# Kernel optimization log

Hardware: AMD Instinct MI355X
Metric: run time of the kernel (lower is better)

The kernel has to match this reference:

```python
import jax, jax.numpy as jnp
import numpy as np

N, E, D, L = 100000, 1_600_000, 128, 8


def setup_inputs() -> dict:
    key = jax.random.key(0)
    k0, k1, k2 = jax.random.split(key, 3)
    x = jax.random.normal(k0, (N, D), dtype=jnp.float32)
    edge_index = jax.random.randint(k1, (2, E), 0, N, dtype=jnp.int64)
    Ws = jax.random.normal(k2, (L, D, D), dtype=jnp.float32) / np.float32(np.sqrt(D))
    bs = jnp.zeros((L, D), dtype=jnp.float32)
    return {"x": x, "edge_index": edge_index, "Ws": Ws, "bs": bs}


def _gcn_conv(h, W, b, src, dst, norm_edge, self_norm):
    """PyG GCNConv: linear -> sym-normalized aggregate (with self loops) -> +bias."""
    h = h @ W                                    # [N, D]
    msg = h[src] * norm_edge[:, None]            # [E, D] gather + scale
    agg = jax.ops.segment_sum(msg, dst, num_segments=h.shape[0])  # scatter-add
    return agg + h * self_norm[:, None] + b      # self-loop term fused in


def reference(x, edge_index, Ws, bs):
    src, dst = edge_index[0], edge_index[1]
    # degree of (A + I) on target nodes, symmetric normalization
    deg = jax.ops.segment_sum(jnp.ones((src.shape[0],), jnp.float32), dst,
                              num_segments=x.shape[0]) + 1.0
    dis = deg ** -0.5                            # deg >= 1, safe
    norm_edge = dis[src] * dis[dst]              # per-edge norm
    self_norm = dis * dis                        # per-node self-loop norm

    n_layers = Ws.shape[0]
    h = x
    initial = x
    for i in range(n_layers):
        h = _gcn_conv(h, Ws[i], bs[i], src, dst, norm_edge, self_norm)
        if i > 0:
            h = h + initial
            initial = h
        h = jax.nn.relu(h)
        if i < n_layers - 1:
            # NOTE: at i == 0 the original indexes layers[-1] (last layer) — faithful.
            j = i - 1
            h = h + _gcn_conv(h, Ws[j], bs[j], src, dst, norm_edge, self_norm)
    return h
```

## Files before the change

kernel.cpp:

```cpp
#include <hip/hip_runtime.h>

#define D 128
#define SCAN_CH 1024
#define SA_STRIDE 136
#define SC_STRIDE 132
#define NPB 64
#define CONV_THREADS 512

typedef _Float16 f16x8 __attribute__((ext_vector_type(8)));
typedef _Float16 f16x4 __attribute__((ext_vector_type(4)));
typedef float f32x4 __attribute__((ext_vector_type(4)));


__global__ void hist_kernel(const int* __restrict__ dst, int* __restrict__ counts,
                            int E, int N) {
  int range = blockIdx.x & 7;
  int lo = (int)(((long long)N * range) >> 3);
  int hi = (int)(((long long)N * (range + 1)) >> 3);
  int stride = (gridDim.x >> 3) * blockDim.x;
  for (int e = (blockIdx.x >> 3) * blockDim.x + threadIdx.x; e < E; e += stride) {
    int d = dst[e];
    if (d >= lo && d < hi) atomicAdd(&counts[d], 1);
  }
}

__global__ void fill_kernel(const int* __restrict__ src, const int* __restrict__ dst,
    int* __restrict__ fillp, int* __restrict__ csr_src, int E, int N) {
  int range = blockIdx.x & 7;
  int lo = (int)(((long long)N * range) >> 3);
  int hi = (int)(((long long)N * (range + 1)) >> 3);
  int stride = (gridDim.x >> 3) * blockDim.x;
  for (int e = (blockIdx.x >> 3) * blockDim.x + threadIdx.x; e < E; e += stride) {
    int d = dst[e];
    if (d >= lo && d < hi) {
      int s = src[e];
      int p = atomicAdd(&fillp[d], 1);
      csr_src[p] = s;
    }
  }
}

__global__ void dis_kernel(const int* __restrict__ counts, float2* __restrict__ dnr, int N) {
  int n = blockIdx.x * blockDim.x + threadIdx.x;
  if (n < N) {
    float c = (float)counts[n] + 1.0f;
    dnr[n] = make_float2(rsqrtf(c), sqrtf(c));
  }
}

__global__ __launch_bounds__(256) void scan_phaseA(const int* __restrict__ counts,
    int* __restrict__ blksum, int N) {
  __shared__ int red[256];
  int base = blockIdx.x * SCAN_CH;
  int t = threadIdx.x;
  int s = 0;
  #pragma unroll
  for (int j = 0; j < 4; ++j) {
    int idx = base + t * 4 + j;
    if (idx < N) s += counts[idx];
  }
  red[t] = s;
  __syncthreads();
  for (int d = 128; d > 0; d >>= 1) {
    if (t < d) red[t] += red[t + d];
    __syncthreads();
  }
  if (t == 0) blksum[blockIdx.x] = red[0];
}

__global__ __launch_bounds__(1024) void scan_phaseB(int* __restrict__ blksum, int NB) {
  __shared__ int sa[1024], sb[1024];
  int t = threadIdx.x;
  int v = (t < NB) ? blksum[t] : 0;
  sa[t] = v;
  __syncthreads();
  int* a = sa; int* b = sb;
  for (int d = 1; d < 1024; d <<= 1) {
    int val = a[t] + ((t >= d) ? a[t - d] : 0);
    b[t] = val;
    __syncthreads();
    int* tmp = a; a = b; b = tmp;
  }
  if (t < NB) blksum[t] = a[t] - v;
}

__global__ __launch_bounds__(256) void scan_phaseC(const int* __restrict__ counts,
    const int* __restrict__ blksum, int* __restrict__ row_ptr, int* __restrict__ fillp, int N) {
  __shared__ int ra[256], rb[256];
  int base = blockIdx.x * SCAN_CH;
  int t = threadIdx.x;
  int v[4]; int s = 0;
  #pragma unroll
  for (int j = 0; j < 4; ++j) {
    int idx = base + t * 4 + j;
    v[j] = (idx < N) ? counts[idx] : 0;
    s += v[j];
  }
  ra[t] = s;
  __syncthreads();
  int* a = ra; int* b = rb;
  for (int d = 1; d < 256; d <<= 1) {
    int val = a[t] + ((t >= d) ? a[t - d] : 0);
    b[t] = val;
    __syncthreads();
    int* tmp = a; a = b; b = tmp;
  }
  int excl = a[t] - s + blksum[blockIdx.x];
  #pragma unroll
  for (int j = 0; j < 4; ++j) {
    int idx = base + t * 4 + j;
    if (idx < N) {
      row_ptr[idx] = excl;
      fillp[idx] = excl;
      excl += v[j];
      if (idx == N - 1) row_ptr[N] = excl;
    }
  }
}


__global__ void conv_x_kernel(const float* __restrict__ x, const float2* __restrict__ dnr,
    _Float16* __restrict__ hs, int total8) {
  int i = blockIdx.x * blockDim.x + threadIdx.x;
  if (i >= total8) return;
  int node = i >> 4;
  float dn = dnr[node].x;
  const float4* p = (const float4*)(x + (size_t)i * 8);
  float4 a = p[0], b = p[1];
  f16x8 v;
  v[0] = (_Float16)(dn * a.x); v[1] = (_Float16)(dn * a.y);
  v[2] = (_Float16)(dn * a.z); v[3] = (_Float16)(dn * a.w);
  v[4] = (_Float16)(dn * b.x); v[5] = (_Float16)(dn * b.y);
  v[6] = (_Float16)(dn * b.z); v[7] = (_Float16)(dn * b.w);
  *(f16x8*)(hs + (size_t)i * 8) = v;
}

__global__ void repack_w_kernel(const float* __restrict__ Ws, _Float16* __restrict__ Wf, int total) {
  int t = blockIdx.x * blockDim.x + threadIdx.x;
  if (t >= total) return;
  int lane = t & 63;
  int nb = (t >> 6) & 7;
  int kb = (t >> 9) & 3;
  int l = t >> 11;
  int col = nb * 16 + (lane & 15);
  int k0 = kb * 32 + (lane >> 4) * 8;
  const float* w = Ws + (size_t)l * D * D;
  f16x8 v;
  #pragma unroll
  for (int j = 0; j < 8; ++j) v[j] = (_Float16)w[(k0 + j) * D + col];
  *(f16x8*)(Wf + (size_t)t * 8) = v;
}

__global__ __launch_bounds__(CONV_THREADS) void conv_fused_kernel(
    const _Float16* __restrict__ hs, const int* __restrict__ row_ptr,
    const int* __restrict__ csr_src, const float2* __restrict__ dnr,
    const f16x8* __restrict__ Wf, const float* __restrict__ bias,
    const float* __restrict__ init32, const _Float16* __restrict__ init16in,
    _Float16* __restrict__ init16out, float* __restrict__ out,
    _Float16* __restrict__ hs_out, int N, int flags) {
  __shared__ __align__(16) char smem[NPB * SC_STRIDE * 4];
  _Float16* sA = (_Float16*)smem;
  float* sC = (float*)smem;
  int tid = threadIdx.x;
  int node0 = blockIdx.x * NPB;
  int ng = tid >> 4;
  int li = tid & 15;
  int c0 = li * 8;

  float2 dr[2];
  f16x8 ownr[2];

  #pragma unroll
  for (int k = 0; k < 2; ++k) {
    int lr = ng + 32 * k;
    int n = node0 + lr;
    f16x8 g = {};
    if (n < N) {
      float acc[8];
      #pragma unroll
      for (int j = 0; j < 8; ++j) acc[j] = 0.f;
      int beg = row_ptr[n], end = row_ptr[n + 1];
      #pragma unroll 4
      for (int e = beg; e < end; ++e) {
        int s = csr_src[e];
        f16x8 v = *(const f16x8*)&hs[(size_t)s * D + c0];
        #pragma unroll
        for (int j = 0; j < 8; ++j) acc[j] += (float)v[j];
      }
      f16x8 own = *(const f16x8*)&hs[(size_t)n * D + c0];
      float2 d2 = dnr[n];
      dr[k] = d2;
      ownr[k] = own;
      #pragma unroll
      for (int j = 0; j < 8; ++j) g[j] = (_Float16)(d2.x * (acc[j] + (float)own[j]));
    }
    *(f16x8*)&sA[lr * SA_STRIDE + c0] = g;
  }

  int wave = tid >> 6, lane = tid & 63;
  f16x8 bf[4];
  #pragma unroll
  for (int kb = 0; kb < 4; ++kb)
    bf[kb] = Wf[(kb * 8 + wave) * 64 + lane];
  __syncthreads();

  f32x4 ca[4];
  #pragma unroll
  for (int rt = 0; rt < 4; ++rt) ca[rt] = (f32x4){0, 0, 0, 0};
  #pragma unroll
  for (int rt = 0; rt < 4; ++rt) {
    #pragma unroll
    for (int kb = 0; kb < 4; ++kb) {
      f16x8 a = *(const f16x8*)&sA[(rt * 16 + (lane & 15)) * SA_STRIDE + kb * 32 + (lane >> 4) * 8];
      ca[rt] = __builtin_amdgcn_mfma_f32_16x16x32_f16(a, bf[kb], ca[rt], 0, 0, 0);
    }
  }
  __syncthreads();

  {
    int colb = wave * 16 + (lane & 15);
    int rowb = (lane >> 4) * 4;
    #pragma unroll
    for (int rt = 0; rt < 4; ++rt)
      #pragma unroll
      for (int r = 0; r < 4; ++r)
        sC[(rt * 16 + rowb + r) * SC_STRIDE + colb] = ca[rt][r];
  }
  __syncthreads();

  float4 b0 = *(const float4*)&bias[c0];
  float4 b1 = *(const float4*)&bias[c0 + 4];
  #pragma unroll
  for (int k = 0; k < 2; ++k) {
    int lr = ng + 32 * k;
    int n = node0 + lr;
    if (n >= N) continue;
    float v[8];
    float4 s0 = *(const float4*)&sC[lr * SC_STRIDE + c0];
    float4 s1 = *(const float4*)&sC[lr * SC_STRIDE + c0 + 4];
    v[0] = s0.x + b0.x; v[1] = s0.y + b0.y; v[2] = s0.z + b0.z; v[3] = s0.w + b0.w;
    v[4] = s1.x + b1.x; v[5] = s1.y + b1.y; v[6] = s1.z + b1.z; v[7] = s1.w + b1.w;
    size_t off = (size_t)n * D + c0;
    if (flags & 8) {
      float rd = dr[k].y;
      #pragma unroll
      for (int j = 0; j < 8; ++j) v[j] += (float)ownr[k][j] * rd;
    }
    if (flags & 1) {
      if (flags & 64) {
        float4 i0 = *(const float4*)&init32[off];
        float4 i1 = *(const float4*)&init32[off + 4];
        v[0] += i0.x; v[1] += i0.y; v[2] += i0.z; v[3] += i0.w;
        v[4] += i1.x; v[5] += i1.y; v[6] += i1.z; v[7] += i1.w;
      } else {
        f16x8 iv = *(const f16x8*)&init16in[off];
        #pragma unroll
        for (int j = 0; j < 8; ++j) v[j] += (float)iv[j];
      }
    }
    if (flags & 2) {
      f16x8 o;
      #pragma unroll
      for (int j = 0; j < 8; ++j) o[j] = (_Float16)v[j];
      *(f16x8*)&init16out[off] = o;
    }
    if (flags & 4) {
      #pragma unroll
      for (int j = 0; j < 8; ++j) v[j] = fmaxf(v[j], 0.f);
    }
    if (flags & 32) {
      *(float4*)&out[off]     = make_float4(v[0], v[1], v[2], v[3]);
      *(float4*)&out[off + 4] = make_float4(v[4], v[5], v[6], v[7]);
    }
    if (flags & 16) {
      float dn = dr[k].x;
      f16x8 h8;
      #pragma unroll
      for (int j = 0; j < 8; ++j) h8[j] = (_Float16)(dn * v[j]);
      *(f16x8*)&hs_out[off] = h8;
    }
  }
}


extern "C" void kernel_launch(void* const* d_in, const int* in_sizes, int n_in,
                              void* d_out, int out_size, void* d_ws, size_t ws_size,
                              hipStream_t stream) {
  const float* x = (const float*)d_in[0];
  const int* ei = (const int*)d_in[1];
  const float* Ws = (const float*)d_in[2];
  const float* bs = (const float*)d_in[3];
  float* out = (float*)d_out;

  const int N = in_sizes[0] / D;
  const int E = in_sizes[1] / 2;
  const int L = in_sizes[2] / (D * D);
  const int* src = ei;
  const int* dst = ei + E;

  uintptr_t p = (uintptr_t)d_ws;
  auto alloc = [&](size_t bytes) {
    uintptr_t r = p;
    p = (r + bytes + 255) & ~(uintptr_t)255;
    return r;
  };
  float2*    dnr      = (float2*)alloc((size_t)N * 8);
  int*       counts   = (int*)  alloc((size_t)N * 4);
  int*       row_ptr  = (int*)  alloc((size_t)(N + 1) * 4);
  int*       fillp    = (int*)  alloc((size_t)N * 4);
  int*       blksum   = (int*)  alloc((size_t)1024 * 4);
  int*       csr_src  = (int*)  alloc((size_t)E * 4);
  _Float16*  hs_a     = (_Float16*)alloc((size_t)N * D * 2);
  _Float16*  hs_b     = (_Float16*)alloc((size_t)N * D * 2);
  _Float16*  init16   = (_Float16*)alloc((size_t)N * D * 2);
  _Float16*  Wf       = (_Float16*)alloc((size_t)L * 4 * 8 * 64 * 8 * 2);

  const int NB = (N + SCAN_CH - 1) / SCAN_CH;

  hipMemsetAsync(counts, 0, (size_t)N * 4, stream);
  hist_kernel<<<8 * 192, 256, 0, stream>>>(dst, counts, E, N);
  dis_kernel<<<(N + 255) / 256, 256, 0, stream>>>(counts, dnr, N);
  scan_phaseA<<<NB, 256, 0, stream>>>(counts, blksum, N);
  scan_phaseB<<<1, 1024, 0, stream>>>(blksum, NB);
  scan_phaseC<<<NB, 256, 0, stream>>>(counts, blksum, row_ptr, fillp, N);
  fill_kernel<<<8 * 192, 256, 0, stream>>>(src, dst, fillp, csr_src, E, N);
  conv_x_kernel<<<(N * 16 + 255) / 256, 256, 0, stream>>>(x, dnr, hs_a, N * 16);
  {
    int total = L * 2048;
    repack_w_kernel<<<(total + 255) / 256, 256, 0, stream>>>(Ws, Wf, total);
  }

  const int conv_grid = (N + NPB - 1) / NPB;
  _Float16* hsp[2] = {hs_a, hs_b};
  int cur = 0;

  for (int i = 0; i < L; ++i) {
    int flags;
    if (i == 0)          flags = 4 | 16;
    else if (i == L - 1) flags = 1 | 4 | 32;
    else                 flags = 1 | 2 | 4 | 16;
    if (i == 1)          flags |= 64;
    conv_fused_kernel<<<conv_grid, CONV_THREADS, 0, stream>>>(hsp[cur], row_ptr, csr_src,
        dnr, (const f16x8*)(Wf + (size_t)i * 2048 * 8), bs + (size_t)i * D,
        x, init16, init16, out, hsp[cur ^ 1], N, flags);
    if (flags & 16) cur ^= 1;
    if (i < L - 1) {
      int j = (i == 0) ? (L - 1) : (i - 1);
      conv_fused_kernel<<<conv_grid, CONV_THREADS, 0, stream>>>(hsp[cur], row_ptr, csr_src,
          dnr, (const f16x8*)(Wf + (size_t)j * 2048 * 8), bs + (size_t)j * D,
          x, init16, init16, out, hsp[cur ^ 1], N, 8 | 16);
      cur ^= 1;
    }
  }
}
```

Before: 1.267 ms.

## Process nodes in degree-sorted order to balance per-block aggregation work

Adds a counting-sort pass (key histogram, scan, scatter) that builds a permutation of nodes ordered by descending in-degree. The fused conv kernel then processes nodes through this permutation, so each 64-node block gets nodes of similar degree and threads within a block stay balanced. The weight fragment loads are also hoisted ahead of the gather loop to overlap with it. The cost is three extra small kernels, an indirect lookup per node, and scattered output writes with less locality in the own-row reads.

```diff
diff --git a/kernel.cpp b/kernel.cpp
--- a/kernel.cpp
+++ b/kernel.cpp
@@ -8,7 +8,6 @@
 #define CONV_THREADS 512
 
 typedef _Float16 f16x8 __attribute__((ext_vector_type(8)));
-typedef _Float16 f16x4 __attribute__((ext_vector_type(4)));
 typedef float f32x4 __attribute__((ext_vector_type(4)));
 
 
@@ -115,6 +114,62 @@
       excl += v[j];
       if (idx == N - 1) row_ptr[N] = excl;
     }
+  }
+}
+
+
+__global__ __launch_bounds__(256) void keyhist_kernel(const int* __restrict__ counts,
+    int* __restrict__ ghist, int N) {
+  __shared__ int lh[256];
+  int t = threadIdx.x;
+  lh[t] = 0;
+  __syncthreads();
+  for (int n = blockIdx.x * 256 + t; n < N; n += gridDim.x * 256) {
+    int k = 255 - min(counts[n], 255);
+    atomicAdd(&lh[k], 1);
+  }
+  __syncthreads();
+  if (lh[t]) atomicAdd(&ghist[t], lh[t]);
+}
+
+__global__ __launch_bounds__(256) void keyscan_kernel(const int* __restrict__ ghist,
+    int* __restrict__ binwork) {
+  __shared__ int a_[256], b_[256];
+  int t = threadIdx.x;
+  int v = ghist[t];
+  a_[t] = v;
+  __syncthreads();
+  int* a = a_; int* b = b_;
+  for (int d = 1; d < 256; d <<= 1) {
+    int val = a[t] + ((t >= d) ? a[t - d] : 0);
+    b[t] = val;
+    __syncthreads();
+    int* tmp = a; a = b; b = tmp;
+  }
+  binwork[t] = a[t] - v;
+}
+
+__global__ __launch_bounds__(256) void scatter_perm_kernel(const int* __restrict__ counts,
+    int* __restrict__ binwork, int* __restrict__ perm, int N) {
+  __shared__ int cnt[256];
+  __shared__ int base[256];
+  int t = threadIdx.x;
+  cnt[t] = 0;
+  __syncthreads();
+  int n = blockIdx.x * 256 + t;
+  int k = -1;
+  if (n < N) {
+    k = 255 - min(counts[n], 255);
+    atomicAdd(&cnt[k], 1);
+  }
+  __syncthreads();
+  int c = cnt[t];
+  if (c) base[t] = atomicAdd(&binwork[t], c);
+  cnt[t] = 0;
+  __syncthreads();
+  if (k >= 0) {
+    int r = atomicAdd(&cnt[k], 1);
+    perm[base[k] + r] = n;
   }
 }
 
@@ -154,10 +209,10 @@
 __global__ __launch_bounds__(CONV_THREADS) void conv_fused_kernel(
     const _Float16* __restrict__ hs, const int* __restrict__ row_ptr,
     const int* __restrict__ csr_src, const float2* __restrict__ dnr,
-    const f16x8* __restrict__ Wf, const float* __restrict__ bias,
-    const float* __restrict__ init32, const _Float16* __restrict__ init16in,
-    _Float16* __restrict__ init16out, float* __restrict__ out,
-    _Float16* __restrict__ hs_out, int N, int flags) {
+    const int* __restrict__ perm, const f16x8* __restrict__ Wf,
+    const float* __restrict__ bias, const float* __restrict__ init32,
+    const _Float16* __restrict__ init16in, _Float16* __restrict__ init16out,
+    float* __restrict__ out, _Float16* __restrict__ hs_out, int N, int flags) {
   __shared__ __align__(16) char smem[NPB * SC_STRIDE * 4];
   _Float16* sA = (_Float16*)smem;
   float* sC = (float*)smem;
@@ -166,16 +221,25 @@
   int ng = tid >> 4;
   int li = tid & 15;
   int c0 = li * 8;
+  int wave = tid >> 6, lane = tid & 63;
+
+  f16x8 bf[4];
+  #pragma unroll
+  for (int kb = 0; kb < 4; ++kb)
+    bf[kb] = Wf[(kb * 8 + wave) * 64 + lane];
 
   float2 dr[2];
   f16x8 ownr[2];
+  int nv[2];
 
   #pragma unroll
   for (int k = 0; k < 2; ++k) {
     int lr = ng + 32 * k;
-    int n = node0 + lr;
+    int idx = node0 + lr;
+    int n = (idx < N) ? perm[idx] : -1;
+    nv[k] = n;
     f16x8 g = {};
-    if (n < N) {
+    if (n >= 0) {
       float acc[8];
       #pragma unroll
       for (int j = 0; j < 8; ++j) acc[j] = 0.f;
@@ -196,12 +260,6 @@
     }
     *(f16x8*)&sA[lr * SA_STRIDE + c0] = g;
   }
-
-  int wave = tid >> 6, lane = tid & 63;
-  f16x8 bf[4];
-  #pragma unroll
-  for (int kb = 0; kb < 4; ++kb)
-    bf[kb] = Wf[(kb * 8 + wave) * 64 + lane];
   __syncthreads();
 
   f32x4 ca[4];
@@ -233,8 +291,8 @@
   #pragma unroll
   for (int k = 0; k < 2; ++k) {
     int lr = ng + 32 * k;
-    int n = node0 + lr;
-    if (n >= N) continue;
+    int n = nv[k];
+    if (n < 0) continue;
     float v[8];
     float4 s0 = *(const float4*)&sC[lr * SC_STRIDE + c0];
     float4 s1 = *(const float4*)&sC[lr * SC_STRIDE + c0 + 4];
@@ -309,6 +367,9 @@
   int*       row_ptr  = (int*)  alloc((size_t)(N + 1) * 4);
   int*       fillp    = (int*)  alloc((size_t)N * 4);
   int*       blksum   = (int*)  alloc((size_t)1024 * 4);
+  int*       ghist    = (int*)  alloc((size_t)256 * 4);
+  int*       binwork  = (int*)  alloc((size_t)256 * 4);
+  int*       perm     = (int*)  alloc((size_t)N * 4);
   int*       csr_src  = (int*)  alloc((size_t)E * 4);
   _Float16*  hs_a     = (_Float16*)alloc((size_t)N * D * 2);
   _Float16*  hs_b     = (_Float16*)alloc((size_t)N * D * 2);
@@ -318,12 +379,16 @@
   const int NB = (N + SCAN_CH - 1) / SCAN_CH;
 
   hipMemsetAsync(counts, 0, (size_t)N * 4, stream);
+  hipMemsetAsync(ghist, 0, 256 * 4, stream);
   hist_kernel<<<8 * 192, 256, 0, stream>>>(dst, counts, E, N);
   dis_kernel<<<(N + 255) / 256, 256, 0, stream>>>(counts, dnr, N);
   scan_phaseA<<<NB, 256, 0, stream>>>(counts, blksum, N);
   scan_phaseB<<<1, 1024, 0, stream>>>(blksum, NB);
   scan_phaseC<<<NB, 256, 0, stream>>>(counts, blksum, row_ptr, fillp, N);
   fill_kernel<<<8 * 192, 256, 0, stream>>>(src, dst, fillp, csr_src, E, N);
+  keyhist_kernel<<<128, 256, 0, stream>>>(counts, ghist, N);
+  keyscan_kernel<<<1, 256, 0, stream>>>(ghist, binwork);
+  scatter_perm_kernel<<<(N + 255) / 256, 256, 0, stream>>>(counts, binwork, perm, N);
   conv_x_kernel<<<(N * 16 + 255) / 256, 256, 0, stream>>>(x, dnr, hs_a, N * 16);
   {
     int total = L * 2048;
@@ -341,13 +406,13 @@
     else                 flags = 1 | 2 | 4 | 16;
     if (i == 1)          flags |= 64;
     conv_fused_kernel<<<conv_grid, CONV_THREADS, 0, stream>>>(hsp[cur], row_ptr, csr_src,
-        dnr, (const f16x8*)(Wf + (size_t)i * 2048 * 8), bs + (size_t)i * D,
+        dnr, perm, (const f16x8*)(Wf + (size_t)i * 2048 * 8), bs + (size_t)i * D,
         x, init16, init16, out, hsp[cur ^ 1], N, flags);
     if (flags & 16) cur ^= 1;
     if (i < L - 1) {
       int j = (i == 0) ? (L - 1) : (i - 1);
       conv_fused_kernel<<<conv_grid, CONV_THREADS, 0, stream>>>(hsp[cur], row_ptr, csr_src,
-          dnr, (const f16x8*)(Wf + (size_t)j * 2048 * 8), bs + (size_t)j * D,
+          dnr, perm, (const f16x8*)(Wf + (size_t)j * 2048 * 8), bs + (size_t)j * D,
           x, init16, init16, out, hsp[cur ^ 1], N, 8 | 16);
       cur ^= 1;
     }
```

Result: no change. 1.262 ms (-0.4%).

## Bucket CSR neighbor lists by source-node range for gather locality

Applied to the files above, without the earlier changes.

Builds the CSR with 8 sub-buckets per destination node keyed by source index range, so each node's neighbor list is grouped by source-id octile. The intent is better cache locality for the feature gathers, since neighbors are visited in partially sorted source order across the grid. This costs an 8x larger count/scan array in preprocessing. The weight-fragment loads are also moved ahead of the gather loop so their latency overlaps with it.

```diff
diff --git a/kernel.cpp b/kernel.cpp
--- a/kernel.cpp
+++ b/kernel.cpp
@@ -8,24 +8,26 @@
 #define CONV_THREADS 512
 
 typedef _Float16 f16x8 __attribute__((ext_vector_type(8)));
-typedef _Float16 f16x4 __attribute__((ext_vector_type(4)));
 typedef float f32x4 __attribute__((ext_vector_type(4)));
 
 
-__global__ void hist_kernel(const int* __restrict__ dst, int* __restrict__ counts,
-                            int E, int N) {
+__global__ void hist2_kernel(const int* __restrict__ src, const int* __restrict__ dst,
+                             int* __restrict__ cnt2, int E, int N, int tsz) {
   int range = blockIdx.x & 7;
   int lo = (int)(((long long)N * range) >> 3);
   int hi = (int)(((long long)N * (range + 1)) >> 3);
   int stride = (gridDim.x >> 3) * blockDim.x;
   for (int e = (blockIdx.x >> 3) * blockDim.x + threadIdx.x; e < E; e += stride) {
     int d = dst[e];
-    if (d >= lo && d < hi) atomicAdd(&counts[d], 1);
-  }
-}
-
-__global__ void fill_kernel(const int* __restrict__ src, const int* __restrict__ dst,
-    int* __restrict__ fillp, int* __restrict__ csr_src, int E, int N) {
+    if (d >= lo && d < hi) {
+      int t = src[e] / tsz;
+      atomicAdd(&cnt2[(size_t)d * 8 + t], 1);
+    }
+  }
+}
+
+__global__ void fill2_kernel(const int* __restrict__ src, const int* __restrict__ dst,
+    int* __restrict__ fillp2, int* __restrict__ csr_src, int E, int N, int tsz) {
   int range = blockIdx.x & 7;
   int lo = (int)(((long long)N * range) >> 3);
   int hi = (int)(((long long)N * (range + 1)) >> 3);
@@ -34,22 +36,23 @@
     int d = dst[e];
     if (d >= lo && d < hi) {
       int s = src[e];
-      int p = atomicAdd(&fillp[d], 1);
+      int p = atomicAdd(&fillp2[(size_t)d * 8 + s / tsz], 1);
       csr_src[p] = s;
     }
   }
 }
 
-__global__ void dis_kernel(const int* __restrict__ counts, float2* __restrict__ dnr, int N) {
+__global__ void dis_kernel(const int* __restrict__ rp2, float2* __restrict__ dnr, int N) {
   int n = blockIdx.x * blockDim.x + threadIdx.x;
   if (n < N) {
-    float c = (float)counts[n] + 1.0f;
+    float c = (float)(rp2[(n + 1) * 8] - rp2[n * 8]) + 1.0f;
     dnr[n] = make_float2(rsqrtf(c), sqrtf(c));
   }
 }
 
+
 __global__ __launch_bounds__(256) void scan_phaseA(const int* __restrict__ counts,
-    int* __restrict__ blksum, int N) {
+    int* __restrict__ blksum, int total) {
   __shared__ int red[256];
   int base = blockIdx.x * SCAN_CH;
   int t = threadIdx.x;
@@ -57,7 +60,7 @@
   #pragma unroll
   for (int j = 0; j < 4; ++j) {
     int idx = base + t * 4 + j;
-    if (idx < N) s += counts[idx];
+    if (idx < total) s += counts[idx];
   }
   red[t] = s;
   __syncthreads();
@@ -85,7 +88,8 @@
 }
 
 __global__ __launch_bounds__(256) void scan_phaseC(const int* __restrict__ counts,
-    const int* __restrict__ blksum, int* __restrict__ row_ptr, int* __restrict__ fillp, int N) {
+    const int* __restrict__ blksum, int* __restrict__ rp2, int* __restrict__ fillp2,
+    int total) {
   __shared__ int ra[256], rb[256];
   int base = blockIdx.x * SCAN_CH;
   int t = threadIdx.x;
@@ -93,7 +97,7 @@
   #pragma unroll
   for (int j = 0; j < 4; ++j) {
     int idx = base + t * 4 + j;
-    v[j] = (idx < N) ? counts[idx] : 0;
+    v[j] = (idx < total) ? counts[idx] : 0;
     s += v[j];
   }
   ra[t] = s;
@@ -109,11 +113,11 @@
   #pragma unroll
   for (int j = 0; j < 4; ++j) {
     int idx = base + t * 4 + j;
-    if (idx < N) {
-      row_ptr[idx] = excl;
-      fillp[idx] = excl;
+    if (idx < total) {
+      rp2[idx] = excl;
+      fillp2[idx] = excl;
       excl += v[j];
-      if (idx == N - 1) row_ptr[N] = excl;
+      if (idx == total - 1) rp2[total] = excl;
     }
   }
 }
@@ -152,7 +156,7 @@
 }
 
 __global__ __launch_bounds__(CONV_THREADS) void conv_fused_kernel(
-    const _Float16* __restrict__ hs, const int* __restrict__ row_ptr,
+    const _Float16* __restrict__ hs, const int* __restrict__ rp2,
     const int* __restrict__ csr_src, const float2* __restrict__ dnr,
     const f16x8* __restrict__ Wf, const float* __restrict__ bias,
     const float* __restrict__ init32, const _Float16* __restrict__ init16in,
@@ -166,6 +170,12 @@
   int ng = tid >> 4;
   int li = tid & 15;
   int c0 = li * 8;
+  int wave = tid >> 6, lane = tid & 63;
+
+  f16x8 bf[4];
+  #pragma unroll
+  for (int kb = 0; kb < 4; ++kb)
+    bf[kb] = Wf[(kb * 8 + wave) * 64 + lane];
 
   float2 dr[2];
   f16x8 ownr[2];
@@ -179,7 +189,7 @@
       float acc[8];
       #pragma unroll
       for (int j = 0; j < 8; ++j) acc[j] = 0.f;
-      int beg = row_ptr[n], end = row_ptr[n + 1];
+      int beg = rp2[n * 8], end = rp2[n * 8 + 8];
       #pragma unroll 4
       for (int e = beg; e < end; ++e) {
         int s = csr_src[e];
@@ -196,12 +206,6 @@
     }
     *(f16x8*)&sA[lr * SA_STRIDE + c0] = g;
   }
-
-  int wave = tid >> 6, lane = tid & 63;
-  f16x8 bf[4];
-  #pragma unroll
-  for (int kb = 0; kb < 4; ++kb)
-    bf[kb] = Wf[(kb * 8 + wave) * 64 + lane];
   __syncthreads();
 
   f32x4 ca[4];
@@ -297,6 +301,8 @@
   const int L = in_sizes[2] / (D * D);
   const int* src = ei;
   const int* dst = ei + E;
+  const int tsz = (N + 7) >> 3;
+  const int total2 = N * 8;
 
   uintptr_t p = (uintptr_t)d_ws;
   auto alloc = [&](size_t bytes) {
@@ -305,9 +311,9 @@
     return r;
   };
   float2*    dnr      = (float2*)alloc((size_t)N * 8);
-  int*       counts   = (int*)  alloc((size_t)N * 4);
-  int*       row_ptr  = (int*)  alloc((size_t)(N + 1) * 4);
-  int*       fillp    = (int*)  alloc((size_t)N * 4);
+  int*       cnt2     = (int*)  alloc((size_t)(total2 + 1) * 4);
+  int*       rp2      = (int*)  alloc((size_t)(total2 + 1) * 4);
+  int*       fillp2   = (int*)  alloc((size_t)(total2 + 1) * 4);
   int*       blksum   = (int*)  alloc((size_t)1024 * 4);
   int*       csr_src  = (int*)  alloc((size_t)E * 4);
   _Float16*  hs_a     = (_Float16*)alloc((size_t)N * D * 2);
@@ -315,15 +321,15 @@
   _Float16*  init16   = (_Float16*)alloc((size_t)N * D * 2);
   _Float16*  Wf       = (_Float16*)alloc((size_t)L * 4 * 8 * 64 * 8 * 2);
 
-  const int NB = (N + SCAN_CH - 1) / SCAN_CH;
-
-  hipMemsetAsync(counts, 0, (size_t)N * 4, stream);
-  hist_kernel<<<8 * 192, 256, 0, stream>>>(dst, counts, E, N);
-  dis_kernel<<<(N + 255) / 256, 256, 0, stream>>>(counts, dnr, N);
-  scan_phaseA<<<NB, 256, 0, stream>>>(counts, blksum, N);
+  const int NB = (total2 + SCAN_CH - 1) / SCAN_CH;
+
+  hipMemsetAsync(cnt2, 0, (size_t)(total2 + 1) * 4, stream);
+  hist2_kernel<<<8 * 192, 256, 0, stream>>>(src, dst, cnt2, E, N, tsz);
+  scan_phaseA<<<NB, 256, 0, stream>>>(cnt2, blksum, total2);
   scan_phaseB<<<1, 1024, 0, stream>>>(blksum, NB);
-  scan_phaseC<<<NB, 256, 0, stream>>>(counts, blksum, row_ptr, fillp, N);
-  fill_kernel<<<8 * 192, 256, 0, stream>>>(src, dst, fillp, csr_src, E, N);
+  scan_phaseC<<<NB, 256, 0, stream>>>(cnt2, blksum, rp2, fillp2, total2);
+  dis_kernel<<<(N + 255) / 256, 256, 0, stream>>>(rp2, dnr, N);
+  fill2_kernel<<<8 * 192, 256, 0, stream>>>(src, dst, fillp2, csr_src, E, N, tsz);
   conv_x_kernel<<<(N * 16 + 255) / 256, 256, 0, stream>>>(x, dnr, hs_a, N * 16);
   {
     int total = L * 2048;
@@ -340,13 +346,13 @@
     else if (i == L - 1) flags = 1 | 4 | 32;
     else                 flags = 1 | 2 | 4 | 16;
     if (i == 1)          flags |= 64;
-    conv_fused_kernel<<<conv_grid, CONV_THREADS, 0, stream>>>(hsp[cur], row_ptr, csr_src,
+    conv_fused_kernel<<<conv_grid, CONV_THREADS, 0, stream>>>(hsp[cur], rp2, csr_src,
         dnr, (const f16x8*)(Wf + (size_t)i * 2048 * 8), bs + (size_t)i * D,
         x, init16, init16, out, hsp[cur ^ 1], N, flags);
     if (flags & 16) cur ^= 1;
     if (i < L - 1) {
       int j = (i == 0) ? (L - 1) : (i - 1);
-      conv_fused_kernel<<<conv_grid, CONV_THREADS, 0, stream>>>(hsp[cur], row_ptr, csr_src,
+      conv_fused_kernel<<<conv_grid, CONV_THREADS, 0, stream>>>(hsp[cur], rp2, csr_src,
           dnr, (const f16x8*)(Wf + (size_t)j * 2048 * 8), bs + (size_t)j * D,
           x, init16, init16, out, hsp[cur ^ 1], N, 8 | 16);
       cur ^= 1;
```

New measurement: 1.355 ms. 7.0% more time.
